# Optimization experiments

Hardware: AMD Instinct MI355X
Metric: run time of the kernel (lower is better)

Reference implementation:

```python
import jax, jax.numpy as jnp
import numpy as np

B, N, E, D, F_IN, EDGE_DIM, VN = 128, 500, 1048576, 128, 5, 2, 10
NEG_FEAT = 0.01   # torch F.leaky_relu default
NEG_ATT = 0.2     # GAT attention slope


def _gat_layer(h_in, src, dst, edge_attr, W, b, a_src, a_dst, a_edge, We, n_nodes):
    # Edge-feature GAT conv: per-edge attention over (src, dst, edge) then
    # softmax-normalized scatter-aggregate onto destination nodes.
    h = h_in @ W                                  # [N, d]
    e = edge_attr @ We                            # [E, d] projected edge features
    logits = jax.nn.leaky_relu((h @ a_src)[src] + (h @ a_dst)[dst] + e @ a_edge,
                               negative_slope=NEG_ATT)    # [E]
    # segment softmax over incoming edges of each dst node
    m = jax.ops.segment_max(logits, dst, num_segments=n_nodes)
    ex = jnp.exp(logits - m[dst])
    denom = jax.ops.segment_sum(ex, dst, num_segments=n_nodes)
    alpha = ex / (denom[dst] + 1e-16)             # [E]
    msg = h[src] + e                              # [E, d]
    out = jax.ops.segment_sum(alpha[:, None] * msg, dst, num_segments=n_nodes)
    return out + b


def setup_inputs() -> dict:
    key = jax.random.key(0)
    ks = jax.random.split(key, 20)
    s = 0.05
    return {
        'x': jax.random.normal(ks[0], (B * N, F_IN), jnp.float32),
        'edge_index': jax.random.randint(ks[1], (2, E), 0, B * N, jnp.int64 if jax.config.jax_enable_x64 else jnp.int32).astype(jnp.int32),
        'edge_attr': jax.random.uniform(ks[2], (E, EDGE_DIM), jnp.float32),
        'curr_v_node_id': jax.random.randint(ks[3], (B,), 0, VN).astype(jnp.int32),
        'v_graph_embedding': jax.random.normal(ks[4], (B, D), jnp.float32),
        'v_node_dense_embeddings': jax.random.normal(ks[5], (B, VN, D), jnp.float32),
        'p_W': jax.random.normal(ks[6], (F_IN, D), jnp.float32) * s,
        'p_b': jnp.zeros((D,), jnp.float32),
        'Ws': jax.random.normal(ks[7], (4, D, D), jnp.float32) * s,
        'bs': jnp.zeros((4, D), jnp.float32),
        'a_srcs': jax.random.normal(ks[8], (4, D), jnp.float32) * s,
        'a_dsts': jax.random.normal(ks[9], (4, D), jnp.float32) * s,
        'a_edges': jax.random.normal(ks[10], (4, D), jnp.float32) * s,
        'Wes': jax.random.normal(ks[11], (4, EDGE_DIM, D), jnp.float32) * s,
        'W5': jax.random.normal(ks[12], (D, 1), jnp.float32) * s,
        'b5': jnp.zeros((1,), jnp.float32),
        'a_src5': jax.random.normal(ks[13], (1,), jnp.float32) * s,
        'a_dst5': jax.random.normal(ks[14], (1,), jnp.float32) * s,
        'a_edge5': jax.random.normal(ks[15], (1,), jnp.float32) * s,
        'We5': jax.random.normal(ks[16], (EDGE_DIM, 1), jnp.float32) * s,
    }


def reference(x, edge_index, edge_attr, curr_v_node_id, v_graph_embedding,
              v_node_dense_embeddings, p_W, p_b, Ws, bs, a_srcs, a_dsts,
              a_edges, Wes, W5, b5, a_src5, a_dst5, a_edge5, We5):
    n_nodes = x.shape[0]
    src, dst = edge_index[0], edge_index[1]
    # gather current v-node embedding: [B, D]
    curr_emb = v_node_dense_embeddings[jnp.arange(B), curr_v_node_id]
    # linear + leaky_relu then broadcast-add of graph/node context
    h = jax.nn.leaky_relu(x @ p_W + p_b, negative_slope=NEG_FEAT)  # [B*N, D]
    h = h.reshape(B, N, D) + v_graph_embedding[:, None, :] + curr_emb[:, None, :]
    h = h.reshape(B * N, D)
    # 4 hidden edge-feature GAT layers (128 -> 128) with leaky_relu
    for l in range(4):
        h = _gat_layer(h, src, dst, edge_attr, Ws[l], bs[l], a_srcs[l],
                       a_dsts[l], a_edges[l], Wes[l], n_nodes)
        h = jax.nn.leaky_relu(h, negative_slope=NEG_FEAT)
    # output layer (128 -> 1), no activation
    h = _gat_layer(h, src, dst, edge_attr, W5, b5, a_src5, a_dst5, a_edge5,
                   We5, n_nodes)                    # [B*N, 1]
    return h.reshape(B, N)
```

## Files before the change

### kernel.cpp

```cpp
#include <hip/hip_runtime.h>
#include <hip/hip_bf16.h>

#define BB   128
#define NN   500
#define NV   64000
#define EE   1048576
#define DD   128
#define FIN  5
#define VNN  10
#define NBUK 250
#define BCAP 8192

typedef unsigned int   uint32;
typedef unsigned short u16b;
typedef __attribute__((ext_vector_type(8))) short short8;
typedef __attribute__((ext_vector_type(4))) float float4v;
typedef __attribute__((ext_vector_type(2))) float float2v;

#define P_ASRC  0
#define P_ADST  512
#define P_WE    1024
#define P_BIAS  2048
#define P_W5    2560
#define P_CVEC  2688
#define P_SC5   2700
#define P_ASD   2816
#define P_TOT   3840

static __device__ __forceinline__ float bf2f(__hip_bfloat16 v) { return __bfloat162float(v); }
static __device__ __forceinline__ float lo2f(uint32 u) { return __uint_as_float(u << 16); }
static __device__ __forceinline__ float hi2f(uint32 u) { return __uint_as_float(u & 0xFFFF0000u); }
static __device__ __forceinline__ uint32 f2bf_bits(float f) {
    uint32 u = __float_as_uint(f);
    return (u + 0x7FFFu + ((u >> 16) & 1u)) >> 16;
}
static __device__ __forceinline__ uint32 pack2(float a, float b) {
    return (f2bf_bits(a) & 0xFFFFu) | (f2bf_bits(b) << 16);
}
static __device__ __forceinline__ float2v unp2(uint32 u) {
    float2v r; r.x = lo2f(u); r.y = hi2f(u); return r;
}
static __device__ __forceinline__ float2v fma2(float2v a, float2v b, float2v c) {
#if __has_builtin(__builtin_elementwise_fma)
    return __builtin_elementwise_fma(a, b, c);
#else
    float2v r; r.x = fmaf(a.x, b.x, c.x); r.y = fmaf(a.y, b.y, c.y); return r;
#endif
}
static __device__ __forceinline__ float2v fma2s(float2v a, float w, float2v c) {
    float2v ww = {w, w};
    return fma2(a, ww, c);
}
static __device__ __forceinline__ float2v shfl_xor2(float2v v, int o) {
    double d; __builtin_memcpy(&d, &v, 8);
    d = __shfl_xor(d, o, 64);
    float2v r; __builtin_memcpy(&r, &d, 8);
    return r;
}
static __device__ __forceinline__ float2v lrelu2(float2v x, float slope) {
    float2v z = {0.f, 0.f};
#if __has_builtin(__builtin_elementwise_max)
    float2v p = __builtin_elementwise_max(x, z);
    float2v q = __builtin_elementwise_min(x, z);
#else
    float2v p; p.x = fmaxf(x.x, 0.f); p.y = fmaxf(x.y, 0.f);
    float2v q; q.x = fminf(x.x, 0.f); q.y = fminf(x.y, 0.f);
#endif
    float2v s = {slope, slope};
    return fma2(q, s, p);
}
static __device__ __forceinline__ float ldf(const void* p, int i, int flag) {
    return flag ? ((const float*)p)[i] : bf2f(((const __hip_bfloat16*)p)[i]);
}

__global__ void sniff_kernel(const unsigned short* __restrict__ p16, int* __restrict__ FLAG) {
    __shared__ int sHigh, sZero;
    if (threadIdx.x == 0) { sHigh = 0; sZero = 0; }
    __syncthreads();
    unsigned short v = p16[2 * threadIdx.x];
    if (v >= 0x8000u) atomicOr(&sHigh, 1);
    if (v == 0)       atomicAdd(&sZero, 1);
    __syncthreads();
    if (threadIdx.x == 0) FLAG[0] = (sHigh || sZero >= 128) ? 1 : 0;
}

__global__ void zero_out_kernel(void* __restrict__ out, const int* __restrict__ FLAG, float tag) {
    int i = blockIdx.x * blockDim.x + threadIdx.x;
    if (i >= NV) return;
    float v = (i == 0) ? tag : 0.f;
    if (FLAG[0]) ((float*)out)[i] = v;
    else         ((u16b*)out)[i] = (u16b)f2bf_bits(v);
}

__global__ void prep_kernel(const void* __restrict__ Wes, const void* __restrict__ aeg,
                            const void* __restrict__ We5, const void* __restrict__ ae5,
                            const void* __restrict__ asr, const void* __restrict__ ads,
                            const void* __restrict__ bs, const void* __restrict__ W5,
                            const void* __restrict__ b5, const void* __restrict__ as5,
                            const void* __restrict__ ad5, const int* __restrict__ FLAG,
                            float* __restrict__ PAR) {
    const int flag = FLAG[0];
    if (blockIdx.x == 0) {
        for (int i = threadIdx.x; i < 512; i += 256) PAR[P_ASRC + i] = ldf(asr, i, flag);
    } else if (blockIdx.x == 1) {
        for (int i = threadIdx.x; i < 512; i += 256) PAR[P_ADST + i] = ldf(ads, i, flag);
    } else if (blockIdx.x == 2) {
        for (int i = threadIdx.x; i < 1024; i += 256) PAR[P_WE + i] = ldf(Wes, i, flag);
    } else if (blockIdx.x == 3) {
        for (int i = threadIdx.x; i < 512; i += 256) PAR[P_BIAS + i] = ldf(bs, i, flag);
    } else if (blockIdx.x == 4) {
        int tid = threadIdx.x;
        if (tid < 128) {
            PAR[P_W5 + tid] = ldf(W5, tid, flag);
        } else if (tid < 136) {
            int l = (tid - 128) >> 1, r = (tid - 128) & 1;
            float s = 0.f;
            for (int ch = 0; ch < DD; ++ch)
                s += ldf(Wes, l * 256 + r * DD + ch, flag) * ldf(aeg, l * DD + ch, flag);
            PAR[P_CVEC + l * 2 + r] = s;
        } else if (tid == 136) {
            float ae = ldf(ae5, 0, flag);
            float w0 = ldf(We5, 0, flag), w1 = ldf(We5, 1, flag);
            PAR[P_CVEC + 8] = w0 * ae; PAR[P_CVEC + 9] = w1 * ae;
            PAR[P_CVEC + 10] = w0;     PAR[P_CVEC + 11] = w1;
            PAR[P_SC5 + 0] = ldf(b5, 0, flag);
            PAR[P_SC5 + 1] = ldf(as5, 0, flag);
            PAR[P_SC5 + 2] = ldf(ad5, 0, flag);
        }
    } else if (blockIdx.x == 5) {
        for (int i = threadIdx.x; i < 512; i += 256) {
            int l = i >> 7, c = i & 127;
            PAR[P_ASD + l * 256 + c * 2]     = ldf(asr, l * DD + c, flag);
            PAR[P_ASD + l * 256 + c * 2 + 1] = ldf(ads, l * DD + c, flag);
        }
    }
}

__global__ __launch_bounds__(256) void prepack_kernel(const void* __restrict__ Ws,
                                                      const int* __restrict__ FLAG,
                                                      u16b* __restrict__ WB) {
    const int flag = FLAG[0];
    int t = blockIdx.x * 256 + threadIdx.x;
    int lane = t & 63;
    int frag = t >> 6;
    int nchunk = frag & 7, kblk = (frag >> 3) & 3, l = frag >> 5;
    int n = nchunk * 16 + (lane & 15);
    int kbase = kblk * 32 + (lane >> 4) * 8;
#pragma unroll
    for (int j = 0; j < 8; ++j) {
        int idx = l * 16384 + (kbase + j) * 128 + n;
        u16b bits = flag ? (u16b)f2bf_bits(((const float*)Ws)[idx])
                         : ((const u16b*)Ws)[idx];
        WB[(size_t)t * 8 + j] = bits;
    }
}

__global__ __launch_bounds__(256) void proj_kernel(
        const void* __restrict__ x, const void* __restrict__ pW,
        const void* __restrict__ pb, const int* __restrict__ curr,
        const void* __restrict__ vge, const void* __restrict__ vnd,
        const int* __restrict__ FLAG, uint32* __restrict__ H) {
    const int flag = FLAG[0];
    const int n = blockIdx.x * 4 + (threadIdx.x >> 6);
    const int lane = threadIdx.x & 63;
    const int b = n / NN;
    int cv = curr[b]; if ((unsigned)cv >= VNN) cv = 0;
    float xv[FIN];
#pragma unroll
    for (int k = 0; k < FIN; ++k) xv[k] = ldf(x, n * FIN + k, flag);
    const int ch = lane * 2;
    float s0 = ldf(pb, ch, flag), s1 = ldf(pb, ch + 1, flag);
#pragma unroll
    for (int k = 0; k < FIN; ++k) {
        s0 = fmaf(xv[k], ldf(pW, k * DD + ch, flag), s0);
        s1 = fmaf(xv[k], ldf(pW, k * DD + ch + 1, flag), s1);
    }
    s0 = (s0 > 0.f) ? s0 : 0.01f * s0;
    s1 = (s1 > 0.f) ? s1 : 0.01f * s1;
    s0 += ldf(vge, b * DD + ch, flag) + ldf(vnd, (b * VNN + cv) * DD + ch, flag);
    s1 += ldf(vge, b * DD + ch + 1, flag) + ldf(vnd, (b * VNN + cv) * DD + ch + 1, flag);
    H[(size_t)n * 64 + lane] = pack2(s0, s1);
}

__global__ void init_kernel(int* __restrict__ gcur, int* __restrict__ counts) {
    int t = blockIdx.x * 256 + threadIdx.x;
    if (t < NBUK) gcur[t] = t * BCAP;
    if (t < 512) counts[NV + t] = 0;
}

__global__ __launch_bounds__(256) void bucketize_kernel(
        const int* __restrict__ src, const int* __restrict__ dst,
        const void* __restrict__ eaP, const int* __restrict__ FLAG,
        int* __restrict__ gcur, uint32* __restrict__ bukx, uint32* __restrict__ buky) {
    __shared__ int cnt[256];
    __shared__ int cur[256];
    const int flag = FLAG[0];
    const int t = threadIdx.x;
    const int e0 = blockIdx.x * 4096;
    cnt[t] = 0;
    __syncthreads();
    int d[16];
#pragma unroll
    for (int i = 0; i < 16; ++i) {
        d[i] = dst[e0 + i * 256 + t];
        if ((unsigned)d[i] >= NV) d[i] = -1;
        if (d[i] >= 0) atomicAdd(&cnt[d[i] >> 8], 1);
    }
    __syncthreads();
    if (t < NBUK) {
        int c = cnt[t];
        cur[t] = c ? atomicAdd(&gcur[t], c) : 0;
    }
    __syncthreads();
#pragma unroll
    for (int i = 0; i < 16; ++i) {
        if (d[i] < 0) continue;
        int e = e0 + i * 256 + t;
        int b = d[i] >> 8;
        int s = src[e];
        if ((unsigned)s >= NV) s = 0;
        uint32 eb;
        if (flag) { float2 v = ((const float2*)eaP)[e]; eb = pack2(v.x, v.y); }
        else      eb = ((const uint32*)eaP)[e];
        int p = atomicAdd(&cur[b], 1);
        if (p < (b + 1) * BCAP) {
            bukx[p] = (uint32)((s & 0xFFFF) | ((d[i] & 255) << 16));
            buky[p] = eb;
        }
    }
}

__global__ __launch_bounds__(256) void bcount_kernel(
        const uint32* __restrict__ bukx, const int* __restrict__ gcur,
        int* __restrict__ counts) {
    __shared__ int c[256];
    const int b = blockIdx.x, t = threadIdx.x;
    c[t] = 0;
    __syncthreads();
    const int base = b * BCAP;
    int cnt = gcur[b] - base;
    if (cnt > BCAP) cnt = BCAP;
    for (int i = t; i < cnt; i += 256)
        atomicAdd(&c[(bukx[base + i] >> 16) & 255], 1);
    __syncthreads();
    counts[b * 256 + t] = c[t];
}

__global__ __launch_bounds__(256) void scan1_kernel(const int* __restrict__ counts,
                                                    int* __restrict__ row_ptr,
                                                    int* __restrict__ partials) {
    __shared__ int sdata[256];
    int tid = threadIdx.x;
    int4 v = ((const int4*)counts)[blockIdx.x * 256 + tid];
    int sum = v.x + v.y + v.z + v.w;
    sdata[tid] = sum;
    __syncthreads();
    int acc = sum;
    for (int off = 1; off < 256; off <<= 1) {
        int t = (tid >= off) ? sdata[tid - off] : 0;
        __syncthreads();
        acc += t;
        sdata[tid] = acc;
        __syncthreads();
    }
    int excl = acc - sum;
    int base = blockIdx.x * 1024 + tid * 4;
    int run = excl;
    if (base + 0 <= NV) row_ptr[base + 0] = run; run += v.x;
    if (base + 1 <= NV) row_ptr[base + 1] = run; run += v.y;
    if (base + 2 <= NV) row_ptr[base + 2] = run; run += v.z;
    if (base + 3 <= NV) row_ptr[base + 3] = run;
    if (tid == 255) partials[blockIdx.x] = acc;
}

__global__ __launch_bounds__(64) void scan2_kernel(const int* __restrict__ partials,
                                                   int* __restrict__ boff, int nb) {
    int lane = threadIdx.x;
    int v = (lane < nb) ? partials[lane] : 0;
    int orig = v;
#pragma unroll
    for (int off = 1; off < 64; off <<= 1) {
        int t = __shfl_up(v, off, 64);
        if (lane >= off) v += t;
    }
    boff[lane] = v - orig;
}

__global__ __launch_bounds__(256) void scan3_kernel(int* __restrict__ row_ptr,
                                                    const int* __restrict__ boff) {
    int add = boff[blockIdx.x];
    int base = blockIdx.x * 1024 + threadIdx.x * 4;
#pragma unroll
    for (int j = 0; j < 4; ++j) {
        int i = base + j;
        if (i <= NV) row_ptr[i] += add;
    }
}

__global__ __launch_bounds__(256) void bscatter_kernel(
        const uint32* __restrict__ bukx, const uint32* __restrict__ buky,
        const int* __restrict__ gcur, const int* __restrict__ row_ptr,
        uint2* __restrict__ csr2) {
    __shared__ int cur[256];
    const int b = blockIdx.x, t = threadIdx.x;
    cur[t] = row_ptr[b * 256 + t];
    __syncthreads();
    const int base = b * BCAP;
    int cnt = gcur[b] - base;
    if (cnt > BCAP) cnt = BCAP;
    for (int i = t; i < cnt; i += 256) {
        uint32 x = bukx[base + i];
        uint32 y = buky[base + i];
        int p = atomicAdd(&cur[(x >> 16) & 255], 1);
        csr2[p] = make_uint2(x & 0xFFFFu, y);
    }
}

__global__ __launch_bounds__(256) void gemm_kernel(
        const uint32* __restrict__ Hu, const u16b* __restrict__ WBl,
        const float* __restrict__ ASDl, uint32* __restrict__ HWu,
        float* __restrict__ ssrc, float* __restrict__ sdst) {
    __shared__ float hs[64 * 129];
    const int tid = threadIdx.x;
    const int lane = tid & 63;
    const int wave = tid >> 6;
    const int quad = lane >> 4;
    const int n0 = blockIdx.x * 64;
    const int m = n0 + wave * 16 + (lane & 15);

    const u16b* hrow = (const u16b*)Hu + (size_t)m * 128;
    short8 a0 = *(const short8*)(hrow + 0  + quad * 8);
    short8 a1 = *(const short8*)(hrow + 32 + quad * 8);
    short8 a2 = *(const short8*)(hrow + 64 + quad * 8);
    short8 a3 = *(const short8*)(hrow + 96 + quad * 8);

    const float2v* asd = (const float2v*)ASDl;
    float2v psd[4];
#pragma unroll
    for (int r = 0; r < 4; ++r) { psd[r].x = 0.f; psd[r].y = 0.f; }

#pragma unroll
    for (int nt = 0; nt < 8; ++nt) {
        const u16b* bbase = WBl + ((size_t)nt * 512 + lane * 8);
        short8 b0 = *(const short8*)(bbase + 0 * 4096);
        short8 b1 = *(const short8*)(bbase + 1 * 4096);
        short8 b2 = *(const short8*)(bbase + 2 * 4096);
        short8 b3 = *(const short8*)(bbase + 3 * 4096);
        float4v acc = {0.f, 0.f, 0.f, 0.f};
        acc = __builtin_amdgcn_mfma_f32_16x16x32_bf16(a0, b0, acc, 0, 0, 0);
        acc = __builtin_amdgcn_mfma_f32_16x16x32_bf16(a1, b1, acc, 0, 0, 0);
        acc = __builtin_amdgcn_mfma_f32_16x16x32_bf16(a2, b2, acc, 0, 0, 0);
        acc = __builtin_amdgcn_mfma_f32_16x16x32_bf16(a3, b3, acc, 0, 0, 0);
        float2v av = asd[nt * 16 + (lane & 15)];
#pragma unroll
        for (int r = 0; r < 4; ++r) {
            hs[(wave * 16 + quad * 4 + r) * 129 + nt * 16 + (lane & 15)] = acc[r];
            psd[r] = fma2s(av, acc[r], psd[r]);
        }
    }
#pragma unroll
    for (int r = 0; r < 4; ++r) {
#pragma unroll
        for (int o = 1; o < 16; o <<= 1) {
            float2v other = shfl_xor2(psd[r], o);
            psd[r].x += other.x; psd[r].y += other.y;
        }
    }
    if ((lane & 15) == 0) {
#pragma unroll
        for (int r = 0; r < 4; ++r) {
            int row = n0 + wave * 16 + quad * 4 + r;
            ssrc[row] = psd[r].x;
            sdst[row] = psd[r].y;
        }
    }
    __syncthreads();

#pragma unroll
    for (int i = 0; i < 4; ++i) {
        int flat = i * 2048 + tid * 8;
        int n = flat >> 7, c = flat & 127;
        const float* p = hs + n * 129 + c;
        uint4 v;
        v.x = pack2(p[0], p[1]); v.y = pack2(p[2], p[3]);
        v.z = pack2(p[4], p[5]); v.w = pack2(p[6], p[7]);
        *(uint4*)(HWu + (size_t)(n0 + n) * 64 + c / 2) = v;
    }
}

__global__ __launch_bounds__(256) void agg_kernel(
        const uint32* __restrict__ HWu, const float* __restrict__ ssrc,
        const float* __restrict__ sdst, const uint2* __restrict__ csr2,
        const int* __restrict__ row_ptr, const float* __restrict__ PAR,
        int layer, uint32* __restrict__ HoutU,
        float* __restrict__ hw5out, int wantw5) {
    __shared__ float exs[4][64];
    const int lane = threadIdx.x & 63;
    const int wid = threadIdx.x >> 6;
    const int n = blockIdx.x * 4 + wid;
    const int begin = __builtin_amdgcn_readfirstlane(row_ptr[n]);
    const int deg   = __builtin_amdgcn_readfirstlane(row_ptr[n + 1]) - begin;
    const float c0 = PAR[P_CVEC + 2 * layer], c1 = PAR[P_CVEC + 2 * layer + 1];
    const float sd = sdst[n];

    int   sv = 0;
    uint32 eb = 0;
    if (lane < deg) {
        uint2 se = csr2[begin + lane];
        sv = (int)se.x;
        eb = se.y;
    }
    const float ssv = ssrc[sv];

    const int dmain = (deg < 64) ? deg : 64;
    const int npad  = (dmain + 15) & ~15;

    uint32 hA[16], hB[16];
#pragma unroll
    for (int q = 0; q < 16; ++q) {
        int s = __builtin_amdgcn_readlane(sv, q);
        hA[q] = HWu[(s << 6) + lane];
    }
    if (npad > 16) {
#pragma unroll
        for (int q = 0; q < 16; ++q) {
            int s = __builtin_amdgcn_readlane(sv, 16 + q);
            hB[q] = HWu[(s << 6) + lane];
        }
    }

    float ex = 0.f;
    if (lane < deg) {
        float L = fmaf(hi2f(eb), c1, fmaf(lo2f(eb), c0, ssv + sd));
        L = (L > 0.f) ? L : 0.2f * L;
        ex = __expf(fminf(L, 60.f));
    }
    exs[wid][lane] = ex;

    float2v acc2 = {0.f, 0.f};
    const float* wp = &exs[wid][0];
#pragma unroll
    for (int q0 = 0; q0 < 16; q0 += 4) {
        float4 w4 = *(const float4*)(wp + q0);
        acc2 = fma2s(unp2(hA[q0 + 0]), w4.x, acc2);
        acc2 = fma2s(unp2(hA[q0 + 1]), w4.y, acc2);
        acc2 = fma2s(unp2(hA[q0 + 2]), w4.z, acc2);
        acc2 = fma2s(unp2(hA[q0 + 3]), w4.w, acc2);
    }
    if (npad > 16) {
#pragma unroll
        for (int q0 = 16; q0 < 32; q0 += 4) {
            float4 w4 = *(const float4*)(wp + q0);
            acc2 = fma2s(unp2(hB[q0 - 16]), w4.x, acc2);
            acc2 = fma2s(unp2(hB[q0 - 15]), w4.y, acc2);
            acc2 = fma2s(unp2(hB[q0 - 14]), w4.z, acc2);
            acc2 = fma2s(unp2(hB[q0 - 13]), w4.w, acc2);
        }
    }
    for (int j = 32; j < dmain; ++j) {
        int s = __builtin_amdgcn_readlane(sv, j);
        float w = wp[j];
        acc2 = fma2s(unp2(HWu[(s << 6) + lane]), w, acc2);
    }

    float dsum = ex;
    float2v sxy = unp2(eb);
    sxy.x *= ex; sxy.y *= ex;
    for (int j0 = 64; j0 < deg; j0 += 64) {
        int j = j0 + lane;
        if (j < deg) {
            uint2 se2 = csr2[begin + j];
            float L2 = fmaf(hi2f(se2.y), c1, fmaf(lo2f(se2.y), c0, ssrc[se2.x] + sd));
            L2 = (L2 > 0.f) ? L2 : 0.2f * L2;
            float x2 = __expf(fminf(L2, 60.f));
            dsum += x2;
            sxy = fma2s(unp2(se2.y), x2, sxy);
        }
    }
#pragma unroll
    for (int o = 32; o; o >>= 1) {
        dsum += __shfl_xor(dsum, o, 64);
        float2v other = shfl_xor2(sxy, o);
        sxy.x += other.x; sxy.y += other.y;
    }

    for (int jj = 64; jj < deg; ++jj) {
        uint2 se2 = csr2[begin + jj];
        float L2 = fmaf(hi2f(se2.y), c1, fmaf(lo2f(se2.y), c0, ssrc[se2.x] + sd));
        L2 = (L2 > 0.f) ? L2 : 0.2f * L2;
        float x2 = __expf(fminf(L2, 60.f));
        acc2 = fma2s(unp2(HWu[(size_t)se2.x * 64 + lane]), x2, acc2);
    }

    const int ch = lane * 2;
    const float* WEl = PAR + P_WE + layer * 256;
    const float inv = __builtin_amdgcn_rcpf(dsum + 1e-16f);
    const float* Bl = PAR + P_BIAS + layer * DD;
    float2v we0 = *(const float2v*)(WEl + ch);
    float2v we1 = *(const float2v*)(WEl + DD + ch);
    float2v bl  = *(const float2v*)(Bl + ch);
    float2v t2 = fma2s(we1, sxy.y, fma2s(we0, sxy.x, acc2));
    float2v o2 = fma2s(t2, inv, bl);
    o2 = lrelu2(o2, 0.01f);
    HoutU[(size_t)n * 64 + lane] = pack2(o2.x, o2.y);

    if (wantw5) {
        float p = o2.x * PAR[P_W5 + ch] + o2.y * PAR[P_W5 + ch + 1];
#pragma unroll
        for (int o = 32; o; o >>= 1) p += __shfl_xor(p, o, 64);
        if (lane == 0) hw5out[n] = p;
    }
}

__global__ __launch_bounds__(256) void final_kernel(
        const float* __restrict__ hw5, const uint2* __restrict__ csr2,
        const int* __restrict__ row_ptr, const float* __restrict__ PAR,
        const int* __restrict__ FLAG, void* __restrict__ out) {
    const int flag = FLAG[0];
    int lane = threadIdx.x & 63;
    int n = blockIdx.x * 4 + (threadIdx.x >> 6);
    int begin = __builtin_amdgcn_readfirstlane(row_ptr[n]);
    int deg   = __builtin_amdgcn_readfirstlane(row_ptr[n + 1]) - begin;
    float c50 = PAR[P_CVEC + 8], c51 = PAR[P_CVEC + 9];
    float ce0 = PAR[P_CVEC + 10], ce1 = PAR[P_CVEC + 11];
    float b5v = PAR[P_SC5], a5s = PAR[P_SC5 + 1];
    float hd = PAR[P_SC5 + 2] * hw5[n];

    float dsum = 0.f, msum = 0.f;
    for (int j0 = 0; j0 < deg; j0 += 64) {
        int j = j0 + lane;
        if (j < deg) {
            uint2 se = csr2[begin + j];
            float hs5 = hw5[se.x];
            float L = fmaf(hi2f(se.y), c51, fmaf(lo2f(se.y), c50, fmaf(a5s, hs5, hd)));
            L = (L > 0.f) ? L : 0.2f * L;
            float ex = __expf(fminf(L, 60.f));
            dsum += ex;
            msum = fmaf(ex, hs5 + fmaf(hi2f(se.y), ce1, lo2f(se.y) * ce0), msum);
        }
    }
#pragma unroll
    for (int o = 32; o; o >>= 1) {
        dsum += __shfl_xor(dsum, o, 64);
        msum += __shfl_xor(msum, o, 64);
    }
    if (lane == 0) {
        float r = msum * __builtin_amdgcn_rcpf(dsum + 1e-16f) + b5v;
        if (flag) ((float*)out)[n] = r;
        else      ((u16b*)out)[n] = (u16b)f2bf_bits(r);
    }
}

extern "C" void kernel_launch(void* const* d_in, const int* in_sizes, int n_in,
                              void* d_out, int out_size, void* d_ws, size_t ws_size,
                              hipStream_t stream) {
    const void* x   = d_in[0];
    const int*  ei  = (const int*)d_in[1];
    const void* ea  = d_in[2];
    const int*  cur = (const int*)d_in[3];
    const void* vge = d_in[4];
    const void* vnd = d_in[5];
    const void* pW  = d_in[6];
    const void* pb  = d_in[7];
    const void* Ws  = d_in[8];
    const void* bs  = d_in[9];
    const void* asr = d_in[10];
    const void* ads = d_in[11];
    const void* aeg = d_in[12];
    const void* Wes = d_in[13];
    const void* W5  = d_in[14];
    const void* b5  = d_in[15];
    const void* as5 = d_in[16];
    const void* ad5 = d_in[17];
    const void* ae5 = d_in[18];
    const void* We5 = d_in[19];
    (void)in_sizes; (void)n_in; (void)out_size;

    const int* e_src = ei;
    const int* e_dst = ei + EE;

    size_t off = 0;
    char* base = (char*)d_ws;
    auto carve = [&](size_t bytes) {
        void* p = base + off;
        off += (bytes + 255) & ~(size_t)255;
        return p;
    };
    int*    FLAG   = (int*)carve(256);
    float*  PAR    = (float*)carve((size_t)P_TOT * 4);
    u16b*   WB     = (u16b*)carve(4 * DD * DD * 2);
    uint32* H0     = (uint32*)carve((size_t)NV * DD * 2);
    uint32* H1     = (uint32*)carve((size_t)NV * DD * 2);
    float*  SS     = (float*)carve(NV * 4);
    float*  SD     = (float*)carve(NV * 4);
    float*  HW5v   = (float*)carve(NV * 4);
    int*    COUNTS = (int*)carve(65536 * 4);
    int*    ROWPTR = (int*)carve(65536 * 4);
    int*    GCUR   = (int*)carve(256 * 4);
    int*    PART   = (int*)carve(256 * 4);
    int*    BOFF   = (int*)carve(256 * 4);
    uint2*  CSR2   = (uint2*)carve((size_t)EE * 8);
    size_t need = off;

    uint32* BUKX = H1;
    uint32* BUKY = H1 + (size_t)NBUK * BCAP;

    sniff_kernel<<<1, 256, 0, stream>>>((const unsigned short*)ea, FLAG);

    if (need > ws_size) {
        zero_out_kernel<<<(NV + 255) / 256, 256, 0, stream>>>(
            d_out, FLAG, (float)(ws_size >> 20));
        return;
    }

    prep_kernel<<<6, 256, 0, stream>>>(Wes, aeg, We5, ae5, asr, ads, bs,
                                       W5, b5, as5, ad5, FLAG, PAR);
    prepack_kernel<<<32, 256, 0, stream>>>(Ws, FLAG, WB);
    proj_kernel<<<NV / 4, 256, 0, stream>>>(x, pW, pb, cur, vge, vnd, FLAG, H0);

    init_kernel<<<2, 256, 0, stream>>>(GCUR, COUNTS);
    bucketize_kernel<<<EE / 4096, 256, 0, stream>>>(e_src, e_dst, ea, FLAG,
                                                    GCUR, BUKX, BUKY);
    bcount_kernel<<<NBUK, 256, 0, stream>>>(BUKX, GCUR, COUNTS);
    scan1_kernel<<<63, 256, 0, stream>>>(COUNTS, ROWPTR, PART);
    scan2_kernel<<<1, 64, 0, stream>>>(PART, BOFF, 63);
    scan3_kernel<<<63, 256, 0, stream>>>(ROWPTR, BOFF);
    bscatter_kernel<<<NBUK, 256, 0, stream>>>(BUKX, BUKY, GCUR, ROWPTR, CSR2);

    for (int l = 0; l < 4; ++l) {
        gemm_kernel<<<NV / 64, 256, 0, stream>>>(
            H0, WB + (size_t)l * 16384, PAR + P_ASD + l * 256, H1, SS, SD);
        agg_kernel<<<NV / 4, 256, 0, stream>>>(
            H1, SS, SD, CSR2, ROWPTR, PAR, l, H0, HW5v, (l == 3) ? 1 : 0);
    }

    final_kernel<<<NV / 4, 256, 0, stream>>>(HW5v, CSR2, ROWPTR, PAR,
                                             FLAG, d_out);
}
```

Baseline: 421.1 us.

## Split aggregation into alpha pass and channel-sliced gather with SoA CSR

The fused per-node aggregation kernel becomes two kernels. The first computes normalized attention weights per edge plus the alpha-weighted edge-attr sums per node. The second does the feature gather in four channel slices, with 16 threads per node and blocks grouped by slice, to improve cache locality of the H rows. The CSR is also split into 16-bit source indices and separate edge-attr words, and the layer-4 w5 projection is accumulated with atomics into a buffer now zeroed in init. This adds an extra launch and alpha writes/reads per layer, and each slice re-reads the indices and alpha.

```diff
diff --git a/kernel.cpp b/kernel.cpp
--- a/kernel.cpp
+++ b/kernel.cpp
@@ -10,6 +10,8 @@
 #define VNN  10
 #define NBUK 250
 #define BCAP 8192
+#define NSLICE 4
+#define NBG  (NV / 16)
 
 typedef unsigned int   uint32;
 typedef unsigned short u16b;
@@ -182,10 +184,12 @@
     H[(size_t)n * 64 + lane] = pack2(s0, s1);
 }
 
-__global__ void init_kernel(int* __restrict__ gcur, int* __restrict__ counts) {
+__global__ void init_kernel(int* __restrict__ gcur, int* __restrict__ counts,
+                            float* __restrict__ hw5) {
     int t = blockIdx.x * 256 + threadIdx.x;
     if (t < NBUK) gcur[t] = t * BCAP;
     if (t < 512) counts[NV + t] = 0;
+    if (t < NV) hw5[t] = 0.f;
 }
 
 __global__ __launch_bounds__(256) void bucketize_kernel(
@@ -300,7 +304,7 @@
 __global__ __launch_bounds__(256) void bscatter_kernel(
         const uint32* __restrict__ bukx, const uint32* __restrict__ buky,
         const int* __restrict__ gcur, const int* __restrict__ row_ptr,
-        uint2* __restrict__ csr2) {
+        u16b* __restrict__ csr_s16, uint32* __restrict__ csr_ea) {
     __shared__ int cur[256];
     const int b = blockIdx.x, t = threadIdx.x;
     cur[t] = row_ptr[b * 256 + t];
@@ -312,7 +316,8 @@
         uint32 x = bukx[base + i];
         uint32 y = buky[base + i];
         int p = atomicAdd(&cur[(x >> 16) & 255], 1);
-        csr2[p] = make_uint2(x & 0xFFFFu, y);
+        csr_s16[p] = (u16b)(x & 0xFFFFu);
+        csr_ea[p]  = y;
     }
 }
 
@@ -388,16 +393,13 @@
     }
 }
 
-__global__ __launch_bounds__(256) void agg_kernel(
-        const uint32* __restrict__ HWu, const float* __restrict__ ssrc,
-        const float* __restrict__ sdst, const uint2* __restrict__ csr2,
+__global__ __launch_bounds__(256) void alpha_kernel(
+        const float* __restrict__ ssrc, const float* __restrict__ sdst,
+        const u16b* __restrict__ csr_s16, const uint32* __restrict__ csr_ea,
         const int* __restrict__ row_ptr, const float* __restrict__ PAR,
-        int layer, uint32* __restrict__ HoutU,
-        float* __restrict__ hw5out, int wantw5) {
-    __shared__ float exs[4][64];
+        int layer, float* __restrict__ alpha, float2* __restrict__ SXY) {
     const int lane = threadIdx.x & 63;
-    const int wid = threadIdx.x >> 6;
-    const int n = blockIdx.x * 4 + wid;
+    const int n = blockIdx.x * 4 + (threadIdx.x >> 6);
     const int begin = __builtin_amdgcn_readfirstlane(row_ptr[n]);
     const int deg   = __builtin_amdgcn_readfirstlane(row_ptr[n + 1]) - begin;
     const float c0 = PAR[P_CVEC + 2 * layer], c1 = PAR[P_CVEC + 2 * layer + 1];
@@ -406,61 +408,16 @@
     int   sv = 0;
     uint32 eb = 0;
     if (lane < deg) {
-        uint2 se = csr2[begin + lane];
-        sv = (int)se.x;
-        eb = se.y;
+        sv = csr_s16[begin + lane];
+        eb = csr_ea[begin + lane];
     }
     const float ssv = ssrc[sv];
-
-    const int dmain = (deg < 64) ? deg : 64;
-    const int npad  = (dmain + 15) & ~15;
-
-    uint32 hA[16], hB[16];
-#pragma unroll
-    for (int q = 0; q < 16; ++q) {
-        int s = __builtin_amdgcn_readlane(sv, q);
-        hA[q] = HWu[(s << 6) + lane];
-    }
-    if (npad > 16) {
-#pragma unroll
-        for (int q = 0; q < 16; ++q) {
-            int s = __builtin_amdgcn_readlane(sv, 16 + q);
-            hB[q] = HWu[(s << 6) + lane];
-        }
-    }
 
     float ex = 0.f;
     if (lane < deg) {
         float L = fmaf(hi2f(eb), c1, fmaf(lo2f(eb), c0, ssv + sd));
         L = (L > 0.f) ? L : 0.2f * L;
         ex = __expf(fminf(L, 60.f));
-    }
-    exs[wid][lane] = ex;
-
-    float2v acc2 = {0.f, 0.f};
-    const float* wp = &exs[wid][0];
-#pragma unroll
-    for (int q0 = 0; q0 < 16; q0 += 4) {
-        float4 w4 = *(const float4*)(wp + q0);
-        acc2 = fma2s(unp2(hA[q0 + 0]), w4.x, acc2);
-        acc2 = fma2s(unp2(hA[q0 + 1]), w4.y, acc2);
-        acc2 = fma2s(unp2(hA[q0 + 2]), w4.z, acc2);
-        acc2 = fma2s(unp2(hA[q0 + 3]), w4.w, acc2);
-    }
-    if (npad > 16) {
-#pragma unroll
-        for (int q0 = 16; q0 < 32; q0 += 4) {
-            float4 w4 = *(const float4*)(wp + q0);
-            acc2 = fma2s(unp2(hB[q0 - 16]), w4.x, acc2);
-            acc2 = fma2s(unp2(hB[q0 - 15]), w4.y, acc2);
-            acc2 = fma2s(unp2(hB[q0 - 14]), w4.z, acc2);
-            acc2 = fma2s(unp2(hB[q0 - 13]), w4.w, acc2);
-        }
-    }
-    for (int j = 32; j < dmain; ++j) {
-        int s = __builtin_amdgcn_readlane(sv, j);
-        float w = wp[j];
-        acc2 = fma2s(unp2(HWu[(s << 6) + lane]), w, acc2);
     }
 
     float dsum = ex;
@@ -469,12 +426,13 @@
     for (int j0 = 64; j0 < deg; j0 += 64) {
         int j = j0 + lane;
         if (j < deg) {
-            uint2 se2 = csr2[begin + j];
-            float L2 = fmaf(hi2f(se2.y), c1, fmaf(lo2f(se2.y), c0, ssrc[se2.x] + sd));
+            int s2 = csr_s16[begin + j];
+            uint32 e2 = csr_ea[begin + j];
+            float L2 = fmaf(hi2f(e2), c1, fmaf(lo2f(e2), c0, ssrc[s2] + sd));
             L2 = (L2 > 0.f) ? L2 : 0.2f * L2;
             float x2 = __expf(fminf(L2, 60.f));
             dsum += x2;
-            sxy = fma2s(unp2(se2.y), x2, sxy);
+            sxy = fma2s(unp2(e2), x2, sxy);
         }
     }
 #pragma unroll
@@ -483,39 +441,91 @@
         float2v other = shfl_xor2(sxy, o);
         sxy.x += other.x; sxy.y += other.y;
     }
-
-    for (int jj = 64; jj < deg; ++jj) {
-        uint2 se2 = csr2[begin + jj];
-        float L2 = fmaf(hi2f(se2.y), c1, fmaf(lo2f(se2.y), c0, ssrc[se2.x] + sd));
-        L2 = (L2 > 0.f) ? L2 : 0.2f * L2;
-        float x2 = __expf(fminf(L2, 60.f));
-        acc2 = fma2s(unp2(HWu[(size_t)se2.x * 64 + lane]), x2, acc2);
-    }
-
-    const int ch = lane * 2;
+    const float inv = __builtin_amdgcn_rcpf(dsum + 1e-16f);
+
+    if (lane < deg) alpha[begin + lane] = ex * inv;
+    for (int j0 = 64; j0 < deg; j0 += 64) {
+        int j = j0 + lane;
+        if (j < deg) {
+            int s2 = csr_s16[begin + j];
+            uint32 e2 = csr_ea[begin + j];
+            float L2 = fmaf(hi2f(e2), c1, fmaf(lo2f(e2), c0, ssrc[s2] + sd));
+            L2 = (L2 > 0.f) ? L2 : 0.2f * L2;
+            alpha[begin + j] = __expf(fminf(L2, 60.f)) * inv;
+        }
+    }
+    if (lane == 0) SXY[n] = make_float2(sxy.x * inv, sxy.y * inv);
+}
+
+__global__ __launch_bounds__(256) void gather_kernel(
+        const uint32* __restrict__ HWu, const float* __restrict__ alpha,
+        const u16b* __restrict__ csr_s16, const int* __restrict__ row_ptr,
+        const float2* __restrict__ SXY, const float* __restrict__ PAR,
+        int layer, uint32* __restrict__ HoutU,
+        float* __restrict__ hw5out, int wantw5) {
+    const int t = threadIdx.x;
+    const int slice = blockIdx.x / NBG;
+    const int nb    = blockIdx.x % NBG;
+    const int g = t >> 4;
+    const int w = t & 15;
+    const int n = nb * 16 + g;
+    const int wordIdx = slice * 16 + w;
+    const int ch = wordIdx * 2;
+
+    const int begin = row_ptr[n];
+    const int deg   = row_ptr[n + 1] - begin;
+
+    float2v acc2 = {0.f, 0.f};
+    int j = 0;
+    for (; j + 4 <= deg; j += 4) {
+        int s0 = csr_s16[begin + j + 0];
+        int s1 = csr_s16[begin + j + 1];
+        int s2 = csr_s16[begin + j + 2];
+        int s3 = csr_s16[begin + j + 3];
+        float a0 = alpha[begin + j + 0];
+        float a1 = alpha[begin + j + 1];
+        float a2 = alpha[begin + j + 2];
+        float a3 = alpha[begin + j + 3];
+        uint32 h0 = HWu[(s0 << 6) + wordIdx];
+        uint32 h1 = HWu[(s1 << 6) + wordIdx];
+        uint32 h2 = HWu[(s2 << 6) + wordIdx];
+        uint32 h3 = HWu[(s3 << 6) + wordIdx];
+        acc2 = fma2s(unp2(h0), a0, acc2);
+        acc2 = fma2s(unp2(h1), a1, acc2);
+        acc2 = fma2s(unp2(h2), a2, acc2);
+        acc2 = fma2s(unp2(h3), a3, acc2);
+    }
+    for (; j < deg; ++j) {
+        int s = csr_s16[begin + j];
+        float a = alpha[begin + j];
+        acc2 = fma2s(unp2(HWu[(s << 6) + wordIdx]), a, acc2);
+    }
+
+    const float2 sxy = SXY[n];
     const float* WEl = PAR + P_WE + layer * 256;
-    const float inv = __builtin_amdgcn_rcpf(dsum + 1e-16f);
-    const float* Bl = PAR + P_BIAS + layer * DD;
+    const float* Bl  = PAR + P_BIAS + layer * DD;
     float2v we0 = *(const float2v*)(WEl + ch);
     float2v we1 = *(const float2v*)(WEl + DD + ch);
     float2v bl  = *(const float2v*)(Bl + ch);
     float2v t2 = fma2s(we1, sxy.y, fma2s(we0, sxy.x, acc2));
-    float2v o2 = fma2s(t2, inv, bl);
+    float2v o2;
+    o2.x = t2.x + bl.x; o2.y = t2.y + bl.y;
     o2 = lrelu2(o2, 0.01f);
-    HoutU[(size_t)n * 64 + lane] = pack2(o2.x, o2.y);
+    HoutU[(size_t)n * 64 + wordIdx] = pack2(o2.x, o2.y);
 
     if (wantw5) {
         float p = o2.x * PAR[P_W5 + ch] + o2.y * PAR[P_W5 + ch + 1];
 #pragma unroll
-        for (int o = 32; o; o >>= 1) p += __shfl_xor(p, o, 64);
-        if (lane == 0) hw5out[n] = p;
+        for (int o = 1; o < 16; o <<= 1) p += __shfl_xor(p, o, 16);
+        if (w == 0) atomicAdd(&hw5out[n], p);
     }
 }
 
 __global__ __launch_bounds__(256) void final_kernel(
-        const float* __restrict__ hw5, const uint2* __restrict__ csr2,
-        const int* __restrict__ row_ptr, const float* __restrict__ PAR,
-        const int* __restrict__ FLAG, void* __restrict__ out) {
+        const float* __restrict__ hw5, const u16b* __restrict__ csr_s16,
+        const uint32* __restrict__ csr_ea, const int* __restrict__ row_ptr,
+        const float* __restrict__ PAR, const int* __restrict__ FLAG,
+        void* __restrict__ out) {
     const int flag = FLAG[0];
     int lane = threadIdx.x & 63;
     int n = blockIdx.x * 4 + (threadIdx.x >> 6);
@@ -530,13 +540,14 @@
     for (int j0 = 0; j0 < deg; j0 += 64) {
         int j = j0 + lane;
         if (j < deg) {
-            uint2 se = csr2[begin + j];
-            float hs5 = hw5[se.x];
-            float L = fmaf(hi2f(se.y), c51, fmaf(lo2f(se.y), c50, fmaf(a5s, hs5, hd)));
+            int s = csr_s16[begin + j];
+            uint32 eb = csr_ea[begin + j];
+            float hs5 = hw5[s];
+            float L = fmaf(hi2f(eb), c51, fmaf(lo2f(eb), c50, fmaf(a5s, hs5, hd)));
             L = (L > 0.f) ? L : 0.2f * L;
             float ex = __expf(fminf(L, 60.f));
             dsum += ex;
-            msum = fmaf(ex, hs5 + fmaf(hi2f(se.y), ce1, lo2f(se.y) * ce0), msum);
+            msum = fmaf(ex, hs5 + fmaf(hi2f(eb), ce1, lo2f(eb) * ce0), msum);
         }
     }
 #pragma unroll
@@ -594,12 +605,15 @@
     float*  SS     = (float*)carve(NV * 4);
     float*  SD     = (float*)carve(NV * 4);
     float*  HW5v   = (float*)carve(NV * 4);
+    float2* SXY    = (float2*)carve((size_t)NV * 8);
     int*    COUNTS = (int*)carve(65536 * 4);
     int*    ROWPTR = (int*)carve(65536 * 4);
     int*    GCUR   = (int*)carve(256 * 4);
     int*    PART   = (int*)carve(256 * 4);
     int*    BOFF   = (int*)carve(256 * 4);
-    uint2*  CSR2   = (uint2*)carve((size_t)EE * 8);
+    u16b*   CSRS16 = (u16b*)carve((size_t)EE * 2);
+    uint32* CSREA  = (uint32*)carve((size_t)EE * 4);
+    float*  ALPHA  = (float*)carve((size_t)EE * 4);
     size_t need = off;
 
     uint32* BUKX = H1;
@@ -618,22 +632,25 @@
     prepack_kernel<<<32, 256, 0, stream>>>(Ws, FLAG, WB);
     proj_kernel<<<NV / 4, 256, 0, stream>>>(x, pW, pb, cur, vge, vnd, FLAG, H0);
 
-    init_kernel<<<2, 256, 0, stream>>>(GCUR, COUNTS);
+    init_kernel<<<NV / 256, 256, 0, stream>>>(GCUR, COUNTS, HW5v);
     bucketize_kernel<<<EE / 4096, 256, 0, stream>>>(e_src, e_dst, ea, FLAG,
                                                     GCUR, BUKX, BUKY);
     bcount_kernel<<<NBUK, 256, 0, stream>>>(BUKX, GCUR, COUNTS);
     scan1_kernel<<<63, 256, 0, stream>>>(COUNTS, ROWPTR, PART);
     scan2_kernel<<<1, 64, 0, stream>>>(PART, BOFF, 63);
     scan3_kernel<<<63, 256, 0, stream>>>(ROWPTR, BOFF);
-    bscatter_kernel<<<NBUK, 256, 0, stream>>>(BUKX, BUKY, GCUR, ROWPTR, CSR2);
+    bscatter_kernel<<<NBUK, 256, 0, stream>>>(BUKX, BUKY, GCUR, ROWPTR,
+                                              CSRS16, CSREA);
 
     for (int l = 0; l < 4; ++l) {
         gemm_kernel<<<NV / 64, 256, 0, stream>>>(
             H0, WB + (size_t)l * 16384, PAR + P_ASD + l * 256, H1, SS, SD);
-        agg_kernel<<<NV / 4, 256, 0, stream>>>(
-            H1, SS, SD, CSR2, ROWPTR, PAR, l, H0, HW5v, (l == 3) ? 1 : 0);
-    }
-
-    final_kernel<<<NV / 4, 256, 0, stream>>>(HW5v, CSR2, ROWPTR, PAR,
+        alpha_kernel<<<NV / 4, 256, 0, stream>>>(
+            SS, SD, CSRS16, CSREA, ROWPTR, PAR, l, ALPHA, SXY);
+        gather_kernel<<<NSLICE * NBG, 256, 0, stream>>>(
+            H1, ALPHA, CSRS16, ROWPTR, SXY, PAR, l, H0, HW5v, (l == 3) ? 1 : 0);
+    }
+
+    final_kernel<<<NV / 4, 256, 0, stream>>>(HW5v, CSRS16, CSREA, ROWPTR, PAR,
                                              FLAG, d_out);
 }
```

New measurement: 613.3 us. +45.6%, slower.

## Fuse GAT aggregation with next layer's GEMM in one kernel

Applied to the files above, without the earlier changes.

Replaces the per-layer agg_kernel + gemm_kernel pair with a fused kernel in which each block aggregates 64 destination nodes into LDS and then runs the next layer's bf16 MFMA projection and attention-score reduction on that tile. This removes one global round trip of the 64000x128 activation per layer and three kernel launches. The SS/SD score buffers are now double-buffered to avoid read/write races. Each block now loops serially over 16 nodes per wave instead of 1, which lowers per-block parallelism and may reduce latency hiding for the irregular gathers.

```diff
diff --git a/kernel.cpp b/kernel.cpp
--- a/kernel.cpp
+++ b/kernel.cpp
@@ -388,127 +388,199 @@
     }
 }
 
-__global__ __launch_bounds__(256) void agg_kernel(
-        const uint32* __restrict__ HWu, const float* __restrict__ ssrc,
+__global__ __launch_bounds__(256, 4) void fused_kernel(
+        const uint32* __restrict__ HWin, const float* __restrict__ ssrc,
         const float* __restrict__ sdst, const uint2* __restrict__ csr2,
         const int* __restrict__ row_ptr, const float* __restrict__ PAR,
-        int layer, uint32* __restrict__ HoutU,
-        float* __restrict__ hw5out, int wantw5) {
+        int layer, const u16b* __restrict__ WBn, const float* __restrict__ ASDn,
+        uint32* __restrict__ HWout, float* __restrict__ ssrc_o,
+        float* __restrict__ sdst_o, float* __restrict__ hw5out, int wantw5) {
+    __shared__ uint32 Hlds[64 * 68];
     __shared__ float exs[4][64];
-    const int lane = threadIdx.x & 63;
-    const int wid = threadIdx.x >> 6;
-    const int n = blockIdx.x * 4 + wid;
-    const int begin = __builtin_amdgcn_readfirstlane(row_ptr[n]);
-    const int deg   = __builtin_amdgcn_readfirstlane(row_ptr[n + 1]) - begin;
+    const int tid = threadIdx.x;
+    const int lane = tid & 63;
+    const int wid = tid >> 6;
+    const int n0 = blockIdx.x * 64;
     const float c0 = PAR[P_CVEC + 2 * layer], c1 = PAR[P_CVEC + 2 * layer + 1];
-    const float sd = sdst[n];
-
-    int   sv = 0;
-    uint32 eb = 0;
-    if (lane < deg) {
-        uint2 se = csr2[begin + lane];
-        sv = (int)se.x;
-        eb = se.y;
-    }
-    const float ssv = ssrc[sv];
-
-    const int dmain = (deg < 64) ? deg : 64;
-    const int npad  = (dmain + 15) & ~15;
-
-    uint32 hA[16], hB[16];
-#pragma unroll
-    for (int q = 0; q < 16; ++q) {
-        int s = __builtin_amdgcn_readlane(sv, q);
-        hA[q] = HWu[(s << 6) + lane];
-    }
-    if (npad > 16) {
+    const int ch = lane * 2;
+    const float* WEl = PAR + P_WE + layer * 256;
+    const float* Bl  = PAR + P_BIAS + layer * DD;
+    const float2v we0 = *(const float2v*)(WEl + ch);
+    const float2v we1 = *(const float2v*)(WEl + DD + ch);
+    const float2v bl  = *(const float2v*)(Bl + ch);
+    float w50 = 0.f, w51 = 0.f;
+    if (wantw5) { w50 = PAR[P_W5 + ch]; w51 = PAR[P_W5 + ch + 1]; }
+
+    for (int i = 0; i < 16; ++i) {
+        const int n = n0 + wid * 16 + i;
+        const int begin = __builtin_amdgcn_readfirstlane(row_ptr[n]);
+        const int deg   = __builtin_amdgcn_readfirstlane(row_ptr[n + 1]) - begin;
+        const float sd = sdst[n];
+
+        int   sv = 0;
+        uint32 eb = 0;
+        if (lane < deg) {
+            uint2 se = csr2[begin + lane];
+            sv = (int)se.x;
+            eb = se.y;
+        }
+        const float ssv = ssrc[sv];
+
+        const int dmain = (deg < 64) ? deg : 64;
+        const int npad  = (dmain + 15) & ~15;
+
+        uint32 hA[16], hB[16];
 #pragma unroll
         for (int q = 0; q < 16; ++q) {
-            int s = __builtin_amdgcn_readlane(sv, 16 + q);
-            hB[q] = HWu[(s << 6) + lane];
-        }
-    }
-
-    float ex = 0.f;
-    if (lane < deg) {
-        float L = fmaf(hi2f(eb), c1, fmaf(lo2f(eb), c0, ssv + sd));
-        L = (L > 0.f) ? L : 0.2f * L;
-        ex = __expf(fminf(L, 60.f));
-    }
-    exs[wid][lane] = ex;
-
-    float2v acc2 = {0.f, 0.f};
-    const float* wp = &exs[wid][0];
-#pragma unroll
-    for (int q0 = 0; q0 < 16; q0 += 4) {
-        float4 w4 = *(const float4*)(wp + q0);
-        acc2 = fma2s(unp2(hA[q0 + 0]), w4.x, acc2);
-        acc2 = fma2s(unp2(hA[q0 + 1]), w4.y, acc2);
-        acc2 = fma2s(unp2(hA[q0 + 2]), w4.z, acc2);
-        acc2 = fma2s(unp2(hA[q0 + 3]), w4.w, acc2);
-    }
-    if (npad > 16) {
-#pragma unroll
-        for (int q0 = 16; q0 < 32; q0 += 4) {
+            int s = __builtin_amdgcn_readlane(sv, q);
+            hA[q] = HWin[(s << 6) + lane];
+        }
+        if (npad > 16) {
+#pragma unroll
+            for (int q = 0; q < 16; ++q) {
+                int s = __builtin_amdgcn_readlane(sv, 16 + q);
+                hB[q] = HWin[(s << 6) + lane];
+            }
+        }
+
+        float ex = 0.f;
+        if (lane < deg) {
+            float L = fmaf(hi2f(eb), c1, fmaf(lo2f(eb), c0, ssv + sd));
+            L = (L > 0.f) ? L : 0.2f * L;
+            ex = __expf(fminf(L, 60.f));
+        }
+        exs[wid][lane] = ex;
+
+        float2v acc2 = {0.f, 0.f};
+        const float* wp = &exs[wid][0];
+#pragma unroll
+        for (int q0 = 0; q0 < 16; q0 += 4) {
             float4 w4 = *(const float4*)(wp + q0);
-            acc2 = fma2s(unp2(hB[q0 - 16]), w4.x, acc2);
-            acc2 = fma2s(unp2(hB[q0 - 15]), w4.y, acc2);
-            acc2 = fma2s(unp2(hB[q0 - 14]), w4.z, acc2);
-            acc2 = fma2s(unp2(hB[q0 - 13]), w4.w, acc2);
-        }
-    }
-    for (int j = 32; j < dmain; ++j) {
-        int s = __builtin_amdgcn_readlane(sv, j);
-        float w = wp[j];
-        acc2 = fma2s(unp2(HWu[(s << 6) + lane]), w, acc2);
-    }
-
-    float dsum = ex;
-    float2v sxy = unp2(eb);
-    sxy.x *= ex; sxy.y *= ex;
-    for (int j0 = 64; j0 < deg; j0 += 64) {
-        int j = j0 + lane;
-        if (j < deg) {
-            uint2 se2 = csr2[begin + j];
+            acc2 = fma2s(unp2(hA[q0 + 0]), w4.x, acc2);
+            acc2 = fma2s(unp2(hA[q0 + 1]), w4.y, acc2);
+            acc2 = fma2s(unp2(hA[q0 + 2]), w4.z, acc2);
+            acc2 = fma2s(unp2(hA[q0 + 3]), w4.w, acc2);
+        }
+        if (npad > 16) {
+#pragma unroll
+            for (int q0 = 16; q0 < 32; q0 += 4) {
+                float4 w4 = *(const float4*)(wp + q0);
+                acc2 = fma2s(unp2(hB[q0 - 16]), w4.x, acc2);
+                acc2 = fma2s(unp2(hB[q0 - 15]), w4.y, acc2);
+                acc2 = fma2s(unp2(hB[q0 - 14]), w4.z, acc2);
+                acc2 = fma2s(unp2(hB[q0 - 13]), w4.w, acc2);
+            }
+        }
+        for (int j = 32; j < dmain; ++j) {
+            int s = __builtin_amdgcn_readlane(sv, j);
+            float w = wp[j];
+            acc2 = fma2s(unp2(HWin[(s << 6) + lane]), w, acc2);
+        }
+
+        float dsum = ex;
+        float2v sxy = unp2(eb);
+        sxy.x *= ex; sxy.y *= ex;
+        for (int j0 = 64; j0 < deg; j0 += 64) {
+            int j = j0 + lane;
+            if (j < deg) {
+                uint2 se2 = csr2[begin + j];
+                float L2 = fmaf(hi2f(se2.y), c1, fmaf(lo2f(se2.y), c0, ssrc[se2.x] + sd));
+                L2 = (L2 > 0.f) ? L2 : 0.2f * L2;
+                float x2 = __expf(fminf(L2, 60.f));
+                dsum += x2;
+                sxy = fma2s(unp2(se2.y), x2, sxy);
+            }
+        }
+#pragma unroll
+        for (int o = 32; o; o >>= 1) {
+            dsum += __shfl_xor(dsum, o, 64);
+            float2v other = shfl_xor2(sxy, o);
+            sxy.x += other.x; sxy.y += other.y;
+        }
+
+        for (int jj = 64; jj < deg; ++jj) {
+            uint2 se2 = csr2[begin + jj];
             float L2 = fmaf(hi2f(se2.y), c1, fmaf(lo2f(se2.y), c0, ssrc[se2.x] + sd));
             L2 = (L2 > 0.f) ? L2 : 0.2f * L2;
             float x2 = __expf(fminf(L2, 60.f));
-            dsum += x2;
-            sxy = fma2s(unp2(se2.y), x2, sxy);
-        }
-    }
-#pragma unroll
-    for (int o = 32; o; o >>= 1) {
-        dsum += __shfl_xor(dsum, o, 64);
-        float2v other = shfl_xor2(sxy, o);
-        sxy.x += other.x; sxy.y += other.y;
-    }
-
-    for (int jj = 64; jj < deg; ++jj) {
-        uint2 se2 = csr2[begin + jj];
-        float L2 = fmaf(hi2f(se2.y), c1, fmaf(lo2f(se2.y), c0, ssrc[se2.x] + sd));
-        L2 = (L2 > 0.f) ? L2 : 0.2f * L2;
-        float x2 = __expf(fminf(L2, 60.f));
-        acc2 = fma2s(unp2(HWu[(size_t)se2.x * 64 + lane]), x2, acc2);
-    }
-
-    const int ch = lane * 2;
-    const float* WEl = PAR + P_WE + layer * 256;
-    const float inv = __builtin_amdgcn_rcpf(dsum + 1e-16f);
-    const float* Bl = PAR + P_BIAS + layer * DD;
-    float2v we0 = *(const float2v*)(WEl + ch);
-    float2v we1 = *(const float2v*)(WEl + DD + ch);
-    float2v bl  = *(const float2v*)(Bl + ch);
-    float2v t2 = fma2s(we1, sxy.y, fma2s(we0, sxy.x, acc2));
-    float2v o2 = fma2s(t2, inv, bl);
-    o2 = lrelu2(o2, 0.01f);
-    HoutU[(size_t)n * 64 + lane] = pack2(o2.x, o2.y);
-
-    if (wantw5) {
-        float p = o2.x * PAR[P_W5 + ch] + o2.y * PAR[P_W5 + ch + 1];
-#pragma unroll
-        for (int o = 32; o; o >>= 1) p += __shfl_xor(p, o, 64);
-        if (lane == 0) hw5out[n] = p;
+            acc2 = fma2s(unp2(HWin[(size_t)se2.x * 64 + lane]), x2, acc2);
+        }
+
+        const float inv = __builtin_amdgcn_rcpf(dsum + 1e-16f);
+        float2v t2 = fma2s(we1, sxy.y, fma2s(we0, sxy.x, acc2));
+        float2v o2 = fma2s(t2, inv, bl);
+        o2 = lrelu2(o2, 0.01f);
+
+        if (wantw5) {
+            float p = o2.x * w50 + o2.y * w51;
+#pragma unroll
+            for (int o = 32; o; o >>= 1) p += __shfl_xor(p, o, 64);
+            if (lane == 0) hw5out[n] = p;
+        } else {
+            Hlds[(wid * 16 + i) * 68 + lane] = pack2(o2.x, o2.y);
+        }
+    }
+    if (wantw5) return;
+
+    const int quad = lane >> 4;
+    const int mloc = wid * 16 + (lane & 15);
+    short8 a0 = *(const short8*)(Hlds + mloc * 68 + 0 * 16 + quad * 4);
+    short8 a1 = *(const short8*)(Hlds + mloc * 68 + 1 * 16 + quad * 4);
+    short8 a2 = *(const short8*)(Hlds + mloc * 68 + 2 * 16 + quad * 4);
+    short8 a3 = *(const short8*)(Hlds + mloc * 68 + 3 * 16 + quad * 4);
+
+    const float2v* asd = (const float2v*)ASDn;
+    float2v psd[4];
+#pragma unroll
+    for (int r = 0; r < 4; ++r) { psd[r].x = 0.f; psd[r].y = 0.f; }
+
+#pragma unroll
+    for (int nt = 0; nt < 8; ++nt) {
+        const u16b* bbase = WBn + ((size_t)nt * 512 + lane * 8);
+        short8 b0 = *(const short8*)(bbase + 0 * 4096);
+        short8 b1 = *(const short8*)(bbase + 1 * 4096);
+        short8 b2 = *(const short8*)(bbase + 2 * 4096);
+        short8 b3 = *(const short8*)(bbase + 3 * 4096);
+        float4v acc = {0.f, 0.f, 0.f, 0.f};
+        acc = __builtin_amdgcn_mfma_f32_16x16x32_bf16(a0, b0, acc, 0, 0, 0);
+        acc = __builtin_amdgcn_mfma_f32_16x16x32_bf16(a1, b1, acc, 0, 0, 0);
+        acc = __builtin_amdgcn_mfma_f32_16x16x32_bf16(a2, b2, acc, 0, 0, 0);
+        acc = __builtin_amdgcn_mfma_f32_16x16x32_bf16(a3, b3, acc, 0, 0, 0);
+        float2v av = asd[nt * 16 + (lane & 15)];
+#pragma unroll
+        for (int r = 0; r < 4; ++r) {
+            psd[r] = fma2s(av, acc[r], psd[r]);
+            float vn = __shfl_xor(acc[r], 1, 64);
+            if (!(lane & 1)) {
+                int row = wid * 16 + quad * 4 + r;
+                Hlds[row * 68 + nt * 8 + ((lane & 15) >> 1)] = pack2(acc[r], vn);
+            }
+        }
+    }
+#pragma unroll
+    for (int r = 0; r < 4; ++r) {
+#pragma unroll
+        for (int o = 1; o < 16; o <<= 1) {
+            float2v other = shfl_xor2(psd[r], o);
+            psd[r].x += other.x; psd[r].y += other.y;
+        }
+    }
+    if ((lane & 15) == 0) {
+#pragma unroll
+        for (int r = 0; r < 4; ++r) {
+            int row = n0 + wid * 16 + quad * 4 + r;
+            ssrc_o[row] = psd[r].x;
+            sdst_o[row] = psd[r].y;
+        }
+    }
+    __syncthreads();
+
+#pragma unroll
+    for (int j = 0; j < 4; ++j) {
+        int flat = j * 1024 + tid * 4;
+        int row = flat >> 6, w = flat & 63;
+        uint4 v = *(const uint4*)(Hlds + row * 68 + w);
+        *(uint4*)(HWout + (size_t)(n0 + row) * 64 + w) = v;
     }
 }
 
@@ -591,8 +663,10 @@
     u16b*   WB     = (u16b*)carve(4 * DD * DD * 2);
     uint32* H0     = (uint32*)carve((size_t)NV * DD * 2);
     uint32* H1     = (uint32*)carve((size_t)NV * DD * 2);
-    float*  SS     = (float*)carve(NV * 4);
-    float*  SD     = (float*)carve(NV * 4);
+    float*  SS0    = (float*)carve(NV * 4);
+    float*  SD0    = (float*)carve(NV * 4);
+    float*  SS1    = (float*)carve(NV * 4);
+    float*  SD1    = (float*)carve(NV * 4);
     float*  HW5v   = (float*)carve(NV * 4);
     int*    COUNTS = (int*)carve(65536 * 4);
     int*    ROWPTR = (int*)carve(65536 * 4);
@@ -627,12 +701,23 @@
     scan3_kernel<<<63, 256, 0, stream>>>(ROWPTR, BOFF);
     bscatter_kernel<<<NBUK, 256, 0, stream>>>(BUKX, BUKY, GCUR, ROWPTR, CSR2);
 
-    for (int l = 0; l < 4; ++l) {
-        gemm_kernel<<<NV / 64, 256, 0, stream>>>(
-            H0, WB + (size_t)l * 16384, PAR + P_ASD + l * 256, H1, SS, SD);
-        agg_kernel<<<NV / 4, 256, 0, stream>>>(
-            H1, SS, SD, CSR2, ROWPTR, PAR, l, H0, HW5v, (l == 3) ? 1 : 0);
-    }
+    gemm_kernel<<<NV / 64, 256, 0, stream>>>(
+        H0, WB, PAR + P_ASD, H1, SS0, SD0);
+    fused_kernel<<<NV / 64, 256, 0, stream>>>(
+        H1, SS0, SD0, CSR2, ROWPTR, PAR, 0,
+        WB + (size_t)1 * 16384, PAR + P_ASD + 1 * 256,
+        H0, SS1, SD1, HW5v, 0);
+    fused_kernel<<<NV / 64, 256, 0, stream>>>(
+        H0, SS1, SD1, CSR2, ROWPTR, PAR, 1,
+        WB + (size_t)2 * 16384, PAR + P_ASD + 2 * 256,
+        H1, SS0, SD0, HW5v, 0);
+    fused_kernel<<<NV / 64, 256, 0, stream>>>(
+        H1, SS0, SD0, CSR2, ROWPTR, PAR, 2,
+        WB + (size_t)3 * 16384, PAR + P_ASD + 3 * 256,
+        H0, SS1, SD1, HW5v, 0);
+    fused_kernel<<<NV / 64, 256, 0, stream>>>(
+        H0, SS1, SD1, CSR2, ROWPTR, PAR, 3,
+        WB, PAR + P_ASD, H1, SS0, SD0, HW5v, 1);
 
     final_kernel<<<NV / 4, 256, 0, stream>>>(HW5v, CSR2, ROWPTR, PAR,
                                              FLAG, d_out);
```

Measured after the change: 420.2 us. No clear change (-0.2%).
